# Kernel optimization log

Measured on AMD Instinct MI355X. Metric: run time of the kernel, lower is better.

Reference implementation:

```python
import jax, jax.numpy as jnp
import numpy as np

NH = 16      # num_heads
D = 128      # head_dim
C = 64       # chunk_size
EPS = 1e-12  # F.normalize eps


def setup_inputs() -> dict:
    key = jax.random.key(0)
    ks = jax.random.split(key, 12)
    B, L, H = 4, 4096, 2048
    std = 0.02
    f32 = jnp.float32
    inp = {
        "hidden_states": jax.random.normal(ks[0], (B, L, H), f32),
        # torch nn.Linear weights are [out_features, in_features]
        "q_w": jax.random.normal(ks[1], (NH * D, H), f32) * std,
        "q_b": jnp.zeros((NH * D,), f32),
        "k_w": jax.random.normal(ks[2], (NH * D, H), f32) * std,
        "k_b": jnp.zeros((NH * D,), f32),
        "v_w": jax.random.normal(ks[3], (NH * D, H), f32) * std,
        "v_b": jnp.zeros((NH * D,), f32),
        "a_w": jax.random.normal(ks[4], (NH, H), f32) * std,
        "a_b": jnp.zeros((NH,), f32),
        "b_w": jax.random.normal(ks[5], (NH, H), f32) * std,
        "b_b": jnp.zeros((NH,), f32),
        "og_w": jax.random.normal(ks[6], (NH * D, H), f32) * std,  # no bias
        "o_w": jax.random.normal(ks[7], (H, NH * D), f32) * std,
        "o_b": jnp.zeros((H,), f32),
    }
    return inp


def _l2norm(x):
    n = jnp.linalg.norm(x, axis=-1, keepdims=True)
    return x / jnp.maximum(n, EPS)


def reference(hidden_states, q_w, q_b, k_w, k_b, v_w, v_b,
              a_w, a_b, b_w, b_b, og_w, o_w, o_b):
    B, L, H = hidden_states.shape
    nh, d, c = NH, D, C
    hs = hidden_states

    q = (hs @ q_w.T + q_b).reshape(B, L, nh, d)
    k = (hs @ k_w.T + k_b).reshape(B, L, nh, d)
    v = (hs @ v_w.T + v_b).reshape(B, L, nh, d)
    # alpha = sigmoid(hs @ a_w.T + a_b) is computed in the original module but
    # never affects the output (alpha_mean / log_alpha are dead code) -> omitted.
    beta = jax.nn.softplus(hs @ b_w.T + b_b)            # [B,L,nh]

    scale = float(d) ** 0.5
    qn = _l2norm(q / scale)                              # normalize makes /scale moot, kept faithful
    kn = _l2norm(k / scale)
    gv = beta[..., None] * v                             # [B,L,nh,d]

    nchunks = L // c

    def to_chunks(x):  # [B,L,nh,d] -> [B,nchunks,nh,c,d]
        return x.reshape(B, nchunks, c, nh, d).transpose(0, 1, 3, 2, 4)

    qc, kc, gvc = to_chunks(qn), to_chunks(kn), to_chunks(gv)

    attn = jnp.einsum('bnhid,bnhjd->bnhij', qc, kc)      # per-chunk QK^T
    pos = jnp.arange(c, dtype=jnp.float32)
    dist = jnp.clip(pos[None, :] - pos[:, None], 0.0, None)   # (j-i) clamped >=0
    decay = jnp.exp(-0.1 * dist)
    causal = pos[None, :] <= pos[:, None]                # keep j<=i, zero j>i
    mask = jnp.where(causal, decay, 0.0)                 # [c,c]
    out = jnp.einsum('bnhij,bnhjd->bnhid', attn * mask, gvc)

    out = out.transpose(0, 1, 3, 2, 4).reshape(B, L, nh * d)
    gate = jax.nn.silu(hs @ og_w.T)                      # output_gate has no bias
    out = out * gate
    return out @ o_w.T + o_b
```

## Files before the change

### kernel.cpp

```cpp
#include <hip/hip_runtime.h>


typedef __bf16 bf16x8 __attribute__((ext_vector_type(8)));
typedef float f32x4 __attribute__((ext_vector_type(4)));

typedef __attribute__((address_space(1))) const unsigned int g_u32;
typedef __attribute__((address_space(3))) unsigned int l_u32;

__device__ __forceinline__ void cp16(const unsigned short* g, unsigned short* l) {
  __builtin_amdgcn_global_load_lds((g_u32*)g, (l_u32*)l, 16, 0, 0);
}

__device__ __forceinline__ unsigned short f2bf(float x) {
  unsigned u = __builtin_bit_cast(unsigned, x);
  u += 0x7fffu + ((u >> 16) & 1u);
  return (unsigned short)(u >> 16);
}
__device__ __forceinline__ float bf2f(unsigned short h) {
  return __builtin_bit_cast(float, (unsigned)h << 16);
}
__device__ __forceinline__ unsigned pk2(float a, float b) {
  return (unsigned)f2bf(a) | ((unsigned)f2bf(b) << 16);
}

__global__ __launch_bounds__(256) void cvt_bf16(const float* __restrict__ in,
                                                unsigned short* __restrict__ out,
                                                int n) {
  int i = (blockIdx.x * 256 + threadIdx.x) * 8;
  if (i >= n) return;
  float4 f0 = *(const float4*)(in + i);
  float4 f1 = *(const float4*)(in + i + 4);
  uint4 u;
  u.x = pk2(f0.x, f0.y); u.y = pk2(f0.z, f0.w);
  u.z = pk2(f1.x, f1.y); u.w = pk2(f1.z, f1.w);
  *(uint4*)(out + i) = u;
}

__global__ __launch_bounds__(256) void build_bias(
    const float* __restrict__ qb, const float* __restrict__ kb,
    const float* __restrict__ vb, float* __restrict__ bias_cat) {
  int i = blockIdx.x * 256 + threadIdx.x;
  float v = 0.f;
  if (i < 2048) v = qb[i];
  else if (i < 4096) v = kb[i - 2048];
  else if (i < 6144) v = vb[i - 4096];
  bias_cat[i] = v;
}

__global__ __launch_bounds__(256) void beta_kernel(
    const float* __restrict__ hs, const float* __restrict__ bw,
    const float* __restrict__ bb, float* __restrict__ beta) {
  __shared__ float row[2048];
  __shared__ float part[16][17];
  const int m = blockIdx.x;
  const float* src = hs + (size_t)m * 2048;
  for (int i = threadIdx.x; i < 512; i += 256)
    ((float4*)row)[i] = ((const float4*)src)[i];
  __syncthreads();
  const int h = threadIdx.x >> 4, j = threadIdx.x & 15;
  const float* w = bw + h * 2048;
  float s = 0.f;
  #pragma unroll 8
  for (int kk = 0; kk < 128; kk++) {
    int k = j + (kk << 4);
    s += row[k] * w[k];
  }
  part[h][j] = s;
  __syncthreads();
  if (threadIdx.x < 16) {
    int hh = threadIdx.x;
    float t = bb[hh];
    #pragma unroll
    for (int j2 = 0; j2 < 16; j2++) t += part[hh][j2];
    beta[(size_t)m * 16 + hh] = fmaxf(t, 0.f) + log1pf(__expf(-fabsf(t)));
  }
}

template <int EPI>
__global__ __launch_bounds__(256) void gemm_async(
    const unsigned short* __restrict__ A, const unsigned short* __restrict__ Bw,
    const float* __restrict__ bias, const float* __restrict__ beta,
    void* __restrict__ Cv, int M, int N, int K) {
  __shared__ __align__(16) unsigned short As[128 * 32];
  __shared__ __align__(16) unsigned short Bs[128 * 32];
  const int tid = threadIdx.x;
  const int m0 = blockIdx.y * 128;
  const int n0 = blockIdx.x * 128;
  const int wid = tid >> 6, lane = tid & 63;
  const int wm = wid >> 1, wn = wid & 1;
  const int quad = lane >> 4, l16 = lane & 15;

  const int srow = tid >> 2;
  const int scol = (tid & 3) << 3;
  const unsigned short* Ag0 = A + (size_t)(m0 + srow) * K + scol;
  const unsigned short* Ag1 = Ag0 + (size_t)64 * K;
  const unsigned short* Bg0 = Bw + (size_t)(n0 + srow) * K + scol;
  const unsigned short* Bg1 = Bg0 + (size_t)64 * K;
  unsigned short* la0 = &As[tid * 8];
  unsigned short* la1 = &As[(tid + 256) * 8];
  unsigned short* lb0 = &Bs[tid * 8];
  unsigned short* lb1 = &Bs[(tid + 256) * 8];

  f32x4 acc[4][4] = {};

  for (int kb = 0; kb < K; kb += 32) {
    cp16(Ag0 + kb, la0);
    cp16(Ag1 + kb, la1);
    cp16(Bg0 + kb, lb0);
    cp16(Bg1 + kb, lb1);
    __syncthreads();
    bf16x8 af[4], bfr[4];
    #pragma unroll
    for (int mi = 0; mi < 4; mi++)
      af[mi] = *(const bf16x8*)&As[(wm * 64 + mi * 16 + l16) * 32 + (quad << 3)];
    #pragma unroll
    for (int ni = 0; ni < 4; ni++)
      bfr[ni] = *(const bf16x8*)&Bs[(wn * 64 + ni * 16 + l16) * 32 + (quad << 3)];
    #pragma unroll
    for (int mi = 0; mi < 4; mi++)
      #pragma unroll
      for (int ni = 0; ni < 4; ni++)
        acc[mi][ni] = __builtin_amdgcn_mfma_f32_16x16x32_bf16(
            af[mi], bfr[ni], acc[mi][ni], 0, 0, 0);
    __syncthreads();
  }

  if (EPI == 0) {
    const int mode = n0 >> 11;
    unsigned short* outp =
        (unsigned short*)Cv + (size_t)mode * ((size_t)M * 2048);
    const int head = (n0 >> 7) & 15;
    #pragma unroll
    for (int mi = 0; mi < 4; mi++) {
      #pragma unroll
      for (int r = 0; r < 4; r++) {
        const int row = m0 + wm * 64 + mi * 16 + quad * 4 + r;
        const float bsc = (mode == 2) ? beta[(size_t)row * 16 + head] : 1.f;
        #pragma unroll
        for (int ni = 0; ni < 4; ni++) {
          const int col = n0 + wn * 64 + ni * 16 + l16;
          float x = acc[mi][ni][r] + bias[col];
          if (mode == 2) x *= bsc;
          if (mode == 3) x = x / (1.f + __expf(-x));
          outp[(size_t)row * 2048 + (col & 2047)] = f2bf(x);
        }
      }
    }
  } else {
    #pragma unroll
    for (int mi = 0; mi < 4; mi++)
      #pragma unroll
      for (int r = 0; r < 4; r++) {
        const int row = m0 + wm * 64 + mi * 16 + quad * 4 + r;
        #pragma unroll
        for (int ni = 0; ni < 4; ni++) {
          const int col = n0 + wn * 64 + ni * 16 + l16;
          ((float*)Cv)[(size_t)row * N + col] = acc[mi][ni][r] + bias[col];
        }
      }
  }
}

constexpr int GLDW = 40;
template <int EPI, bool ABF16>
__global__ __launch_bounds__(256) void gemm_bt(
    const void* __restrict__ Av, const float* __restrict__ Bw,
    const float* __restrict__ bias, const float* __restrict__ beta,
    void* __restrict__ Cv, int M, int N, int K) {
  __shared__ unsigned short As[128 * GLDW];
  __shared__ unsigned short Bs[128 * GLDW];
  const int tid = threadIdx.x;
  const int m0 = blockIdx.y * 128;
  const int n0 = blockIdx.x * 128;
  const int wid = tid >> 6, lane = tid & 63;
  const int wm = wid >> 1, wn = wid & 1;
  const int quad = lane >> 4, l16 = lane & 15;
  const int srow = tid >> 1, skh = (tid & 1) << 4;

  f32x4 acc[4][4] = {};
  const float* Bg = Bw + (size_t)(n0 + srow) * K + skh;

  for (int kb = 0; kb < K; kb += 32) {
    if (ABF16) {
      const unsigned short* Ag =
          (const unsigned short*)Av + (size_t)(m0 + srow) * K + kb + skh;
      uint4 u0 = ((const uint4*)Ag)[0];
      uint4 u1 = ((const uint4*)Ag)[1];
      uint4* d = (uint4*)&As[srow * GLDW + skh];
      d[0] = u0; d[1] = u1;
    } else {
      const float* Ag = (const float*)Av + (size_t)(m0 + srow) * K + kb + skh;
      float4 f0 = ((const float4*)Ag)[0];
      float4 f1 = ((const float4*)Ag)[1];
      float4 f2 = ((const float4*)Ag)[2];
      float4 f3 = ((const float4*)Ag)[3];
      unsigned* d = (unsigned*)&As[srow * GLDW + skh];
      d[0] = pk2(f0.x, f0.y); d[1] = pk2(f0.z, f0.w);
      d[2] = pk2(f1.x, f1.y); d[3] = pk2(f1.z, f1.w);
      d[4] = pk2(f2.x, f2.y); d[5] = pk2(f2.z, f2.w);
      d[6] = pk2(f3.x, f3.y); d[7] = pk2(f3.z, f3.w);
    }
    {
      const float* Bgk = Bg + kb;
      float4 f0 = ((const float4*)Bgk)[0];
      float4 f1 = ((const float4*)Bgk)[1];
      float4 f2 = ((const float4*)Bgk)[2];
      float4 f3 = ((const float4*)Bgk)[3];
      unsigned* d = (unsigned*)&Bs[srow * GLDW + skh];
      d[0] = pk2(f0.x, f0.y); d[1] = pk2(f0.z, f0.w);
      d[2] = pk2(f1.x, f1.y); d[3] = pk2(f1.z, f1.w);
      d[4] = pk2(f2.x, f2.y); d[5] = pk2(f2.z, f2.w);
      d[6] = pk2(f3.x, f3.y); d[7] = pk2(f3.z, f3.w);
    }
    __syncthreads();
    bf16x8 af[4], bfr[4];
    #pragma unroll
    for (int mi = 0; mi < 4; mi++)
      af[mi] = *(const bf16x8*)&As[(wm * 64 + mi * 16 + l16) * GLDW + (quad << 3)];
    #pragma unroll
    for (int ni = 0; ni < 4; ni++)
      bfr[ni] = *(const bf16x8*)&Bs[(wn * 64 + ni * 16 + l16) * GLDW + (quad << 3)];
    #pragma unroll
    for (int mi = 0; mi < 4; mi++)
      #pragma unroll
      for (int ni = 0; ni < 4; ni++)
        acc[mi][ni] = __builtin_amdgcn_mfma_f32_16x16x32_bf16(
            af[mi], bfr[ni], acc[mi][ni], 0, 0, 0);
    __syncthreads();
  }

  #pragma unroll
  for (int mi = 0; mi < 4; mi++) {
    #pragma unroll
    for (int r = 0; r < 4; r++) {
      const int row = m0 + wm * 64 + mi * 16 + quad * 4 + r;
      float bsc = 1.f;
      if (EPI == 1) bsc = beta[(size_t)row * 16 + blockIdx.x];
      #pragma unroll
      for (int ni = 0; ni < 4; ni++) {
        const int col = n0 + wn * 64 + ni * 16 + l16;
        float x = acc[mi][ni][r];
        if (EPI != 2) x += bias[col];
        if (EPI == 1) x *= bsc;
        if (EPI == 2) x = x / (1.f + __expf(-x));
        if (EPI == 3)
          ((float*)Cv)[(size_t)row * N + col] = x;
        else
          ((unsigned short*)Cv)[(size_t)row * N + col] = f2bf(x);
      }
    }
  }
}

constexpr int QK_LDW = 136;
constexpr int GT_LDW = 72;
constexpr int SS_LDW = 72;

__global__ __launch_bounds__(256) void attn_kernel(
    const unsigned short* __restrict__ qn, const unsigned short* __restrict__ kn,
    const unsigned short* __restrict__ gvp, const unsigned short* __restrict__ gate,
    unsigned short* __restrict__ y) {
  __shared__ unsigned short qs[64 * QK_LDW];
  __shared__ unsigned short ks[64 * QK_LDW];
  __shared__ unsigned short gst[128 * GT_LDW];
  __shared__ unsigned short Ss[64 * SS_LDW];

  const int tid = threadIdx.x;
  const int m0 = blockIdx.x * 64;
  const int h = blockIdx.y;
  const size_t gbase = (size_t)m0 * 2048 + (size_t)h * 128;

  #pragma unroll
  for (int it = 0; it < 4; it++) {
    int e = tid + it * 256;
    int i = e >> 4;
    int c = (e & 15) << 3;
    size_t g = gbase + (size_t)i * 2048 + c;
    *(uint4*)&qs[i * QK_LDW + c] = *(const uint4*)&qn[g];
    *(uint4*)&ks[i * QK_LDW + c] = *(const uint4*)&kn[g];
    uint4 gvv = *(const uint4*)&gvp[g];
    unsigned short tmp[8];
    *(uint4*)tmp = gvv;
    #pragma unroll
    for (int t = 0; t < 8; t++) gst[(c + t) * GT_LDW + i] = tmp[t];
  }
  __syncthreads();

  {
    const int rr = tid >> 2;
    const int seg = (tid & 3) * 32;
    float ssq = 0.f, ssk = 0.f;
    #pragma unroll
    for (int k2 = 0; k2 < 32; k2 += 2) {
      unsigned uq = *(const unsigned*)&qs[rr * QK_LDW + seg + k2];
      unsigned uk = *(const unsigned*)&ks[rr * QK_LDW + seg + k2];
      float a = bf2f((unsigned short)(uq & 0xffff)), b = bf2f((unsigned short)(uq >> 16));
      float c2 = bf2f((unsigned short)(uk & 0xffff)), d2 = bf2f((unsigned short)(uk >> 16));
      ssq += a * a + b * b;
      ssk += c2 * c2 + d2 * d2;
    }
    ssq += __shfl_xor(ssq, 1); ssq += __shfl_xor(ssq, 2);
    ssk += __shfl_xor(ssk, 1); ssk += __shfl_xor(ssk, 2);
    float iq = rsqrtf(fmaxf(ssq, 1e-24f));
    float ik = rsqrtf(fmaxf(ssk, 1e-24f));
    #pragma unroll
    for (int k2 = 0; k2 < 32; k2 += 2) {
      unsigned uq = *(const unsigned*)&qs[rr * QK_LDW + seg + k2];
      unsigned uk = *(const unsigned*)&ks[rr * QK_LDW + seg + k2];
      float a = bf2f((unsigned short)(uq & 0xffff)), b = bf2f((unsigned short)(uq >> 16));
      float c2 = bf2f((unsigned short)(uk & 0xffff)), d2 = bf2f((unsigned short)(uk >> 16));
      *(unsigned*)&qs[rr * QK_LDW + seg + k2] = pk2(a * iq, b * iq);
      *(unsigned*)&ks[rr * QK_LDW + seg + k2] = pk2(c2 * ik, d2 * ik);
    }
  }
  __syncthreads();

  const int w = tid >> 6;
  const int lane = tid & 63;
  const int quad = lane >> 4, l16 = lane & 15;

  {
    f32x4 acc[4] = {};
    #pragma unroll
    for (int kst = 0; kst < 4; kst++) {
      bf16x8 a = *(const bf16x8*)&qs[(w * 16 + l16) * QK_LDW + kst * 32 + (quad << 3)];
      #pragma unroll
      for (int ni = 0; ni < 4; ni++) {
        bf16x8 b = *(const bf16x8*)&ks[(ni * 16 + l16) * QK_LDW + kst * 32 + (quad << 3)];
        acc[ni] = __builtin_amdgcn_mfma_f32_16x16x32_bf16(a, b, acc[ni], 0, 0, 0);
      }
    }
    #pragma unroll
    for (int ni = 0; ni < 4; ni++)
      #pragma unroll
      for (int r = 0; r < 4; r++) {
        int row = w * 16 + quad * 4 + r;
        int col = ni * 16 + l16;
        float val = (col <= row) ? acc[ni][r] : 0.f;
        Ss[row * SS_LDW + col] = f2bf(val);
      }
  }
  __syncthreads();

  {
    f32x4 acc[8] = {};
    #pragma unroll
    for (int kst = 0; kst < 2; kst++) {
      bf16x8 a = *(const bf16x8*)&Ss[(w * 16 + l16) * SS_LDW + kst * 32 + (quad << 3)];
      #pragma unroll
      for (int nd = 0; nd < 8; nd++) {
        bf16x8 b = *(const bf16x8*)&gst[(nd * 16 + l16) * GT_LDW + kst * 32 + (quad << 3)];
        acc[nd] = __builtin_amdgcn_mfma_f32_16x16x32_bf16(a, b, acc[nd], 0, 0, 0);
      }
    }
    #pragma unroll
    for (int nd = 0; nd < 8; nd++)
      #pragma unroll
      for (int r = 0; r < 4; r++) {
        int row = w * 16 + quad * 4 + r;
        int col = nd * 16 + l16;
        size_t g = gbase + (size_t)row * 2048 + col;
        float gt = bf2f(gate[g]);
        y[g] = f2bf(acc[nd][r] * gt);
      }
  }
}

extern "C" void kernel_launch(void* const* d_in, const int* in_sizes, int n_in,
                              void* d_out, int out_size, void* d_ws, size_t ws_size,
                              hipStream_t stream) {
  const float* hs   = (const float*)d_in[0];
  const float* q_w  = (const float*)d_in[1];
  const float* q_b  = (const float*)d_in[2];
  const float* k_w  = (const float*)d_in[3];
  const float* k_b  = (const float*)d_in[4];
  const float* v_w  = (const float*)d_in[5];
  const float* v_b  = (const float*)d_in[6];
  const float* b_w  = (const float*)d_in[9];
  const float* b_b  = (const float*)d_in[10];
  const float* og_w = (const float*)d_in[11];
  const float* o_w  = (const float*)d_in[12];
  const float* o_b  = (const float*)d_in[13];

  const int M = 16384, K = 2048;
  const size_t MB64 = 67108864;

  const size_t OFF_HSB  = 4 * MB64;
  const size_t OFF_WCAT = OFF_HSB + MB64;
  const size_t OFF_OWB  = OFF_WCAT + 33554432;
  const size_t OFF_BETA = OFF_OWB + 8388608;
  const size_t OFF_BIAS = OFF_BETA + 1048576;
  const size_t NEED     = OFF_BIAS + 32768;

  char* ws = (char*)d_ws;

  if (ws_size >= NEED) {
    unsigned short* qy   = (unsigned short*)ws;
    unsigned short* knb  = (unsigned short*)(ws + MB64);
    unsigned short* gv   = (unsigned short*)(ws + 2 * MB64);
    unsigned short* gate = (unsigned short*)(ws + 3 * MB64);
    unsigned short* hsb  = (unsigned short*)(ws + OFF_HSB);
    unsigned short* wcat = (unsigned short*)(ws + OFF_WCAT);
    unsigned short* owb  = (unsigned short*)(ws + OFF_OWB);
    float*          beta = (float*)(ws + OFF_BETA);
    float*          bias = (float*)(ws + OFF_BIAS);

    const int NW = 4194304;
    cvt_bf16<<<(M * K) / 2048, 256, 0, stream>>>(hs, hsb, M * K);
    cvt_bf16<<<NW / 2048, 256, 0, stream>>>(q_w,  wcat,          NW);
    cvt_bf16<<<NW / 2048, 256, 0, stream>>>(k_w,  wcat + NW,     NW);
    cvt_bf16<<<NW / 2048, 256, 0, stream>>>(v_w,  wcat + 2 * NW, NW);
    cvt_bf16<<<NW / 2048, 256, 0, stream>>>(og_w, wcat + 3 * NW, NW);
    cvt_bf16<<<NW / 2048, 256, 0, stream>>>(o_w,  owb,           NW);
    build_bias<<<32, 256, 0, stream>>>(q_b, k_b, v_b, bias);
    beta_kernel<<<M, 256, 0, stream>>>(hs, b_w, b_b, beta);

    gemm_async<0><<<dim3(64, 128), 256, 0, stream>>>(
        hsb, wcat, bias, beta, qy, M, 8192, K);

    attn_kernel<<<dim3(256, 16), 256, 0, stream>>>(qy, knb, gv, gate, qy);

    gemm_async<3><<<dim3(16, 128), 256, 0, stream>>>(
        qy, owb, o_b, nullptr, (float*)d_out, M, 2048, K);
  } else {
    unsigned short* qy   = (unsigned short*)ws;
    unsigned short* knb  = (unsigned short*)(ws + MB64);
    unsigned short* gv   = (unsigned short*)(ws + 2 * MB64);
    unsigned short* gate = (unsigned short*)(ws + 3 * MB64);
    float*          beta = (float*)(ws + 4 * MB64);

    beta_kernel<<<M, 256, 0, stream>>>(hs, b_w, b_b, beta);
    dim3 gg(16, 128);
    gemm_bt<0, false><<<gg, 256, 0, stream>>>(hs, q_w, q_b, nullptr, qy, M, 2048, K);
    gemm_bt<0, false><<<gg, 256, 0, stream>>>(hs, k_w, k_b, nullptr, knb, M, 2048, K);
    gemm_bt<1, false><<<gg, 256, 0, stream>>>(hs, v_w, v_b, beta, gv, M, 2048, K);
    gemm_bt<2, false><<<gg, 256, 0, stream>>>(hs, og_w, nullptr, nullptr, gate, M, 2048, K);
    attn_kernel<<<dim3(256, 16), 256, 0, stream>>>(qy, knb, gv, gate, qy);
    gemm_bt<3, true><<<gg, 256, 0, stream>>>(qy, o_w, o_b, nullptr, (float*)d_out, M, 2048, K);
  }
}
```

Baseline: 1.420 ms.

## Fuse activation bf16 conversion into beta kernel and swizzle GEMM LDS tiles

The beta kernel now also writes the bf16 copy of hidden_states from the row it already holds in shared memory, which removes a separate conversion launch and a second read of the activations. The async GEMM gets an XOR swizzle on its LDS load and store column chunks to cut bank conflicts, and it now takes N and K as template constants with a launch-bounds occupancy hint of 4. The attention kernel's LDS row paddings are also changed. Together these aim to cut memory traffic, LDS conflicts and address arithmetic, at the risk of higher register pressure from the occupancy hint and new bank conflicts from the altered padding.

```diff
diff --git a/kernel.cpp b/kernel.cpp
--- a/kernel.cpp
+++ b/kernel.cpp
@@ -49,7 +49,8 @@
 
 __global__ __launch_bounds__(256) void beta_kernel(
     const float* __restrict__ hs, const float* __restrict__ bw,
-    const float* __restrict__ bb, float* __restrict__ beta) {
+    const float* __restrict__ bb, float* __restrict__ beta,
+    unsigned short* __restrict__ hsb) {
   __shared__ float row[2048];
   __shared__ float part[16][17];
   const int m = blockIdx.x;
@@ -57,6 +58,13 @@
   for (int i = threadIdx.x; i < 512; i += 256)
     ((float4*)row)[i] = ((const float4*)src)[i];
   __syncthreads();
+  if (hsb) {
+    int e = threadIdx.x * 8;
+    uint4 u;
+    u.x = pk2(row[e], row[e + 1]);     u.y = pk2(row[e + 2], row[e + 3]);
+    u.z = pk2(row[e + 4], row[e + 5]); u.w = pk2(row[e + 6], row[e + 7]);
+    *(uint4*)(hsb + (size_t)m * 2048 + e) = u;
+  }
   const int h = threadIdx.x >> 4, j = threadIdx.x & 15;
   const float* w = bw + h * 2048;
   float s = 0.f;
@@ -76,11 +84,11 @@
   }
 }
 
-template <int EPI>
-__global__ __launch_bounds__(256) void gemm_async(
+template <int EPI, int N, int K>
+__global__ __launch_bounds__(256, 4) void gemm_async(
     const unsigned short* __restrict__ A, const unsigned short* __restrict__ Bw,
     const float* __restrict__ bias, const float* __restrict__ beta,
-    void* __restrict__ Cv, int M, int N, int K) {
+    void* __restrict__ Cv) {
   __shared__ __align__(16) unsigned short As[128 * 32];
   __shared__ __align__(16) unsigned short Bs[128 * 32];
   const int tid = threadIdx.x;
@@ -91,7 +99,7 @@
   const int quad = lane >> 4, l16 = lane & 15;
 
   const int srow = tid >> 2;
-  const int scol = (tid & 3) << 3;
+  const int scol = ((tid & 3) ^ ((tid >> 3) & 3)) << 3;
   const unsigned short* Ag0 = A + (size_t)(m0 + srow) * K + scol;
   const unsigned short* Ag1 = Ag0 + (size_t)64 * K;
   const unsigned short* Bg0 = Bw + (size_t)(n0 + srow) * K + scol;
@@ -101,6 +109,8 @@
   unsigned short* lb0 = &Bs[tid * 8];
   unsigned short* lb1 = &Bs[(tid + 256) * 8];
 
+  const int pchunk = (quad ^ ((l16 >> 1) & 3)) << 3;
+
   f32x4 acc[4][4] = {};
 
   for (int kb = 0; kb < K; kb += 32) {
@@ -112,10 +122,10 @@
     bf16x8 af[4], bfr[4];
     #pragma unroll
     for (int mi = 0; mi < 4; mi++)
-      af[mi] = *(const bf16x8*)&As[(wm * 64 + mi * 16 + l16) * 32 + (quad << 3)];
+      af[mi] = *(const bf16x8*)&As[(wm * 64 + mi * 16 + l16) * 32 + pchunk];
     #pragma unroll
     for (int ni = 0; ni < 4; ni++)
-      bfr[ni] = *(const bf16x8*)&Bs[(wn * 64 + ni * 16 + l16) * 32 + (quad << 3)];
+      bfr[ni] = *(const bf16x8*)&Bs[(wn * 64 + ni * 16 + l16) * 32 + pchunk];
     #pragma unroll
     for (int mi = 0; mi < 4; mi++)
       #pragma unroll
@@ -128,7 +138,7 @@
   if (EPI == 0) {
     const int mode = n0 >> 11;
     unsigned short* outp =
-        (unsigned short*)Cv + (size_t)mode * ((size_t)M * 2048);
+        (unsigned short*)Cv + (size_t)mode * ((size_t)16384 * 2048);
     const int head = (n0 >> 7) & 15;
     #pragma unroll
     for (int mi = 0; mi < 4; mi++) {
@@ -252,9 +262,9 @@
   }
 }
 
-constexpr int QK_LDW = 136;
-constexpr int GT_LDW = 72;
-constexpr int SS_LDW = 72;
+constexpr int QK_LDW = 132;
+constexpr int GT_LDW = 66;
+constexpr int SS_LDW = 68;
 
 __global__ __launch_bounds__(256) void attn_kernel(
     const unsigned short* __restrict__ qn, const unsigned short* __restrict__ kn,
@@ -406,22 +416,21 @@
     float*          bias = (float*)(ws + OFF_BIAS);
 
     const int NW = 4194304;
-    cvt_bf16<<<(M * K) / 2048, 256, 0, stream>>>(hs, hsb, M * K);
     cvt_bf16<<<NW / 2048, 256, 0, stream>>>(q_w,  wcat,          NW);
     cvt_bf16<<<NW / 2048, 256, 0, stream>>>(k_w,  wcat + NW,     NW);
     cvt_bf16<<<NW / 2048, 256, 0, stream>>>(v_w,  wcat + 2 * NW, NW);
     cvt_bf16<<<NW / 2048, 256, 0, stream>>>(og_w, wcat + 3 * NW, NW);
     cvt_bf16<<<NW / 2048, 256, 0, stream>>>(o_w,  owb,           NW);
     build_bias<<<32, 256, 0, stream>>>(q_b, k_b, v_b, bias);
-    beta_kernel<<<M, 256, 0, stream>>>(hs, b_w, b_b, beta);
-
-    gemm_async<0><<<dim3(64, 128), 256, 0, stream>>>(
-        hsb, wcat, bias, beta, qy, M, 8192, K);
+    beta_kernel<<<M, 256, 0, stream>>>(hs, b_w, b_b, beta, hsb);
+
+    gemm_async<0, 8192, 2048><<<dim3(64, 128), 256, 0, stream>>>(
+        hsb, wcat, bias, beta, qy);
 
     attn_kernel<<<dim3(256, 16), 256, 0, stream>>>(qy, knb, gv, gate, qy);
 
-    gemm_async<3><<<dim3(16, 128), 256, 0, stream>>>(
-        qy, owb, o_b, nullptr, (float*)d_out, M, 2048, K);
+    gemm_async<3, 2048, 2048><<<dim3(16, 128), 256, 0, stream>>>(
+        qy, owb, o_b, nullptr, (float*)d_out);
   } else {
     unsigned short* qy   = (unsigned short*)ws;
     unsigned short* knb  = (unsigned short*)(ws + MB64);
@@ -429,7 +438,7 @@
     unsigned short* gate = (unsigned short*)(ws + 3 * MB64);
     float*          beta = (float*)(ws + 4 * MB64);
 
-    beta_kernel<<<M, 256, 0, stream>>>(hs, b_w, b_b, beta);
+    beta_kernel<<<M, 256, 0, stream>>>(hs, b_w, b_b, beta, nullptr);
     dim3 gg(16, 128);
     gemm_bt<0, false><<<gg, 256, 0, stream>>>(hs, q_w, q_b, nullptr, qy, M, 2048, K);
     gemm_bt<0, false><<<gg, 256, 0, stream>>>(hs, k_w, k_b, nullptr, knb, M, 2048, K);
```

New measurement: 1.272 ms. 10.5% less time.
